# Kernel optimization log

Hardware: AMD Instinct MI355X
Metric: run time of the kernel (lower is better)

The kernel has to match this reference:

```python
import jax, jax.numpy as jnp
import numpy as np
from jax import lax

B, L, H = 32, 512, 1024
PRED_LEN = 32
LN_EPS = 1e-5


def setup_inputs() -> dict:
    key = jax.random.key(0)
    k1, k2, k3 = jax.random.split(key, 3)
    x = jax.random.normal(k1, (B, L, H), dtype=jnp.float32)
    # scale recurrent/input weights by 1/sqrt(H) so the linear recurrence stays finite
    Wxh = jax.random.normal(k2, (H, H), dtype=jnp.float32) / jnp.sqrt(jnp.float32(H))
    Whh = jax.random.normal(k3, (H, H), dtype=jnp.float32) / jnp.sqrt(jnp.float32(H))
    ln_w = jnp.ones((H,), dtype=jnp.float32)
    ln_b = jnp.zeros((H,), dtype=jnp.float32)
    return {"x": x, "Wxh": Wxh, "Whh": Whh, "ln_w": ln_w, "ln_b": ln_b, "pred_len": PRED_LEN}


def _layer_norm(y, w, b):
    mu = jnp.mean(y, axis=-1, keepdims=True)
    var = jnp.mean(jnp.square(y - mu), axis=-1, keepdims=True)
    return (y - mu) * lax.rsqrt(var + LN_EPS) * w + b


def reference(x, Wxh, Whh, ln_w, ln_b, pred_len):
    b, l, h = x.shape
    # precompute input projections for all timesteps: x_t @ Wxh^T (nn.Linear convention)
    xW = jnp.einsum('blh,kh->lbk', x, Wxh)  # [L, B, H]
    WhhT = Whh.T

    def rec_step(h_t, xw_t):
        h_t = xw_t + h_t @ WhhT
        return h_t, h_t

    h0 = jnp.zeros((b, h), dtype=x.dtype)
    h_last, rec = lax.scan(rec_step, h0, xW)
    rec = jnp.transpose(rec, (1, 0, 2))  # [B, L, H]

    def pred_step(h_t, _):
        h_t = h_t @ WhhT
        return h_t, h_t

    _, outs = lax.scan(pred_step, h_last, None, length=pred_len)
    outs = jnp.transpose(outs, (1, 0, 2))  # [B, pred_len, H]
    outputs = _layer_norm(outs, ln_w, ln_b)
    return rec, outputs
```

## Files before the change

### kernel.cpp

```cpp
#include <hip/hip_runtime.h>

#define BB 32
#define LL 512
#define HH 1024
#define PRED 32
#define C8 8
#define NC8 (LL / C8)
#define LN_EPS 1e-5f

typedef short bf16x8 __attribute__((ext_vector_type(8)));
typedef short s16x4  __attribute__((ext_vector_type(4)));
typedef float f32x4  __attribute__((ext_vector_type(4)));

static __device__ __forceinline__ void split3(float x, short& h, short& m, short& l) {
    unsigned u = __float_as_uint(x);
    unsigned rh = (u + 0x7fffu + ((u >> 16) & 1u)) & 0xffff0000u;
    h = (short)(rh >> 16);
    float x1 = x - __uint_as_float(rh);
    unsigned u1 = __float_as_uint(x1);
    unsigned rm = (u1 + 0x7fffu + ((u1 >> 16) & 1u)) & 0xffff0000u;
    m = (short)(rm >> 16);
    float x2 = x1 - __uint_as_float(rm);
    unsigned u2 = __float_as_uint(x2);
    unsigned rl = (u2 + 0x7fffu + ((u2 >> 16) & 1u)) & 0xffff0000u;
    l = (short)(rl >> 16);
}

static __device__ __forceinline__ void split2(float x, short& h, short& m) {
    unsigned u = __float_as_uint(x);
    unsigned rh = (u + 0x7fffu + ((u >> 16) & 1u)) & 0xffff0000u;
    h = (short)(rh >> 16);
    float x1 = x - __uint_as_float(rh);
    unsigned u1 = __float_as_uint(x1);
    unsigned rm = (u1 + 0x7fffu + ((u1 >> 16) & 1u)) & 0xffff0000u;
    m = (short)(rm >> 16);
}

#define MFMA6(ACC, AH, AM, AL, BH, BM, BL) \
    ACC = __builtin_amdgcn_mfma_f32_16x16x32_bf16(AL, BH, ACC, 0, 0, 0); \
    ACC = __builtin_amdgcn_mfma_f32_16x16x32_bf16(AH, BL, ACC, 0, 0, 0); \
    ACC = __builtin_amdgcn_mfma_f32_16x16x32_bf16(AM, BM, ACC, 0, 0, 0); \
    ACC = __builtin_amdgcn_mfma_f32_16x16x32_bf16(AM, BH, ACC, 0, 0, 0); \
    ACC = __builtin_amdgcn_mfma_f32_16x16x32_bf16(AH, BM, ACC, 0, 0, 0); \
    ACC = __builtin_amdgcn_mfma_f32_16x16x32_bf16(AH, BH, ACC, 0, 0, 0);

__global__ __launch_bounds__(256) void transpose_k(const float* __restrict__ in,
                                                   float* __restrict__ out) {
    __shared__ float tile[32][33];
    int bx = blockIdx.x * 32, by = blockIdx.y * 32;
    int tx = threadIdx.x, ty = threadIdx.y;
    #pragma unroll
    for (int i = 0; i < 32; i += 8)
        tile[ty + i][tx] = in[(size_t)(by + ty + i) * HH + bx + tx];
    __syncthreads();
    #pragma unroll
    for (int i = 0; i < 32; i += 8)
        out[(size_t)(bx + ty + i) * HH + by + tx] = tile[tx][ty + i];
}

__global__ __launch_bounds__(256) void split_a(const float* __restrict__ src, long sb, long sc,
                                               short* __restrict__ dst, long dsb, long dsc,
                                               long ps) {
    int r = blockIdx.y;
    const float* s = src + (long)(r & 31) * sb + (long)(r >> 5) * sc + threadIdx.x * 4;
    short* d = dst + (long)(r & 31) * dsb + (long)(r >> 5) * dsc + threadIdx.x * 4;
    float4 v = *(const float4*)s;
    float xs[4] = {v.x, v.y, v.z, v.w};
    s16x4 vh, vm, vl;
    #pragma unroll
    for (int j = 0; j < 4; ++j) {
        short h, m, l;
        split3(xs[j], h, m, l);
        vh[j] = h; vm[j] = m; vl[j] = l;
    }
    *(s16x4*)(d) = vh;
    *(s16x4*)(d + ps) = vm;
    *(s16x4*)(d + 2 * ps) = vl;
}

__global__ __launch_bounds__(256) void split_t(const float* __restrict__ in,
                                               short* __restrict__ out) {
    const size_t HM = (size_t)HH * HH;
    __shared__ float tile[32][33];
    int n0 = blockIdx.x * 32, k0 = blockIdx.y * 32;
    int tx = threadIdx.x, ty = threadIdx.y;
    #pragma unroll
    for (int i = 0; i < 32; i += 8)
        tile[ty + i][tx] = in[(size_t)(k0 + ty + i) * HH + n0 + tx];
    __syncthreads();
    #pragma unroll
    for (int i = 0; i < 32; i += 8) {
        float v = tile[tx][ty + i];
        short h, m, l;
        split3(v, h, m, l);
        size_t o = (size_t)(n0 + ty + i) * HH + k0 + tx;
        out[o] = h; out[HM + o] = m; out[2 * HM + o] = l;
    }
}

__global__ __launch_bounds__(256) void tr_splits(const short* __restrict__ in,
                                                 short* __restrict__ out) {
    const size_t HM = (size_t)HH * HH;
    __shared__ short tile[32][33];
    int p = blockIdx.z;
    int k0 = blockIdx.x * 32, n0 = blockIdx.y * 32;
    int tx = threadIdx.x, ty = threadIdx.y;
    #pragma unroll
    for (int i = 0; i < 32; i += 8)
        tile[ty + i][tx] = in[p * HM + (size_t)(n0 + ty + i) * HH + k0 + tx];
    __syncthreads();
    #pragma unroll
    for (int i = 0; i < 32; i += 8)
        out[p * HM + (size_t)(k0 + ty + i) * HH + n0 + tx] = tile[tx][ty + i];
}

__global__ __launch_bounds__(256) void copy_splits(const short* __restrict__ src,
                                                   short* __restrict__ dst, long ps) {
    size_t off = (size_t)blockIdx.x * HH + threadIdx.x * 4;
    *(s16x4*)(dst + off)          = *(const s16x4*)(src + off);
    *(s16x4*)(dst + ps + off)     = *(const s16x4*)(src + ps + off);
    *(s16x4*)(dst + 2 * ps + off) = *(const s16x4*)(src + 2 * ps + off);
}

__global__ __launch_bounds__(256) void gemm_mx(const float* __restrict__ A,
                                               const short* __restrict__ SB,
                                               float* __restrict__ C) {
    const size_t HM = (size_t)HH * HH;
    __shared__ __align__(16) short As2[2][128][40];
    __shared__ __align__(16) short Bs2[2][64][40];
    const int tid = threadIdx.x;
    const int lane = tid & 63;
    const int w = tid >> 6;
    const int n0 = blockIdx.x * 64;
    const int m0 = blockIdx.y * 128;
    const int ar = tid >> 1;
    const int akc = (tid & 1) * 16;
    const float* Arow = A + (size_t)(m0 + ar) * HH + akc;
    const int bp = tid >> 7;
    const int bnr = tid & 63;
    const int bkh = ((tid >> 6) & 1) * 16;
    const short* Brow = SB + bp * HM + (size_t)(n0 + bnr) * HH + bkh;
    const int fr = lane & 15;
    const int fk = (lane >> 4) * 8;

    f32x4 acc[2][4] = {};

    float4 av0 = *(const float4*)(Arow);
    float4 av1 = *(const float4*)(Arow + 4);
    float4 av2 = *(const float4*)(Arow + 8);
    float4 av3 = *(const float4*)(Arow + 12);
    bf16x8 rb0 = *(const bf16x8*)(Brow);
    bf16x8 rb1 = *(const bf16x8*)(Brow + 8);

    for (int kt = 0; kt < HH; kt += 32) {
        float xs[16] = {av0.x, av0.y, av0.z, av0.w, av1.x, av1.y, av1.z, av1.w,
                        av2.x, av2.y, av2.z, av2.w, av3.x, av3.y, av3.z, av3.w};
        bf16x8 vh0, vm0, vh1, vm1;
        #pragma unroll
        for (int j = 0; j < 8; ++j) {
            short h, m;
            split2(xs[j], h, m);
            vh0[j] = h; vm0[j] = m;
            split2(xs[j + 8], h, m);
            vh1[j] = h; vm1[j] = m;
        }
        *(bf16x8*)&As2[0][ar][akc]     = vh0;
        *(bf16x8*)&As2[0][ar][akc + 8] = vh1;
        *(bf16x8*)&As2[1][ar][akc]     = vm0;
        *(bf16x8*)&As2[1][ar][akc + 8] = vm1;
        *(bf16x8*)&Bs2[bp][bnr][bkh]     = rb0;
        *(bf16x8*)&Bs2[bp][bnr][bkh + 8] = rb1;
        __syncthreads();
        if (kt + 32 < HH) {
            const float* An = Arow + kt + 32;
            av0 = *(const float4*)(An);
            av1 = *(const float4*)(An + 4);
            av2 = *(const float4*)(An + 8);
            av3 = *(const float4*)(An + 12);
            const short* Bn = Brow + kt + 32;
            rb0 = *(const bf16x8*)(Bn);
            rb1 = *(const bf16x8*)(Bn + 8);
        }
        bf16x8 ah[2], am[2];
        #pragma unroll
        for (int i = 0; i < 2; ++i) {
            ah[i] = *(const bf16x8*)&As2[0][w * 32 + i * 16 + fr][fk];
            am[i] = *(const bf16x8*)&As2[1][w * 32 + i * 16 + fr][fk];
        }
        #pragma unroll
        for (int j = 0; j < 4; ++j) {
            bf16x8 bh = *(const bf16x8*)&Bs2[0][j * 16 + fr][fk];
            bf16x8 bm = *(const bf16x8*)&Bs2[1][j * 16 + fr][fk];
            #pragma unroll
            for (int i = 0; i < 2; ++i) {
                f32x4 a = acc[i][j];
                a = __builtin_amdgcn_mfma_f32_16x16x32_bf16(am[i], bm, a, 0, 0, 0);
                a = __builtin_amdgcn_mfma_f32_16x16x32_bf16(am[i], bh, a, 0, 0, 0);
                a = __builtin_amdgcn_mfma_f32_16x16x32_bf16(ah[i], bm, a, 0, 0, 0);
                a = __builtin_amdgcn_mfma_f32_16x16x32_bf16(ah[i], bh, a, 0, 0, 0);
                acc[i][j] = a;
            }
        }
        __syncthreads();
    }
    const int orow = (lane >> 4) * 4;
    #pragma unroll
    for (int i = 0; i < 2; ++i)
        #pragma unroll
        for (int j = 0; j < 4; ++j) {
            int c = n0 + j * 16 + fr;
            #pragma unroll
            for (int reg = 0; reg < 4; ++reg) {
                int r = m0 + w * 32 + i * 16 + orow + reg;
                C[(size_t)r * HH + c] = acc[i][j][reg];
            }
        }
}

struct GD  { const short* A; const short* B; float* O; float* P; short* S; };
struct GD8 { GD g[8]; };

__global__ __launch_bounds__(256) void step_b(
    GD8 dsc, int ypg,
    long sab, long sac, long psA,
    long sob, long soc, int add,
    long spb, long spc,
    long ssb, long ssc, long psS,
    int nrows) {
    const size_t HM = (size_t)HH * HH;
    __shared__ __align__(16) short As[3][128][40];
    __shared__ __align__(16) short Bs[3][64][40];
    const int tid = threadIdx.x;
    const int lane = tid & 63;
    const int w = tid >> 6;
    const int grp = blockIdx.y / ypg;
    const int yy  = blockIdx.y % ypg;
    const int n0 = blockIdx.x * 64;
    const int m0 = yy * 128;
    const GD d = dsc.g[grp];
    const int ar = tid >> 1;
    const int akh = (tid & 1) * 16;
    const int agr = m0 + ar;
    const short* Arow = d.A + (long)(agr & 31) * sab + (long)(agr >> 5) * sac + akh;
    const int br = tid >> 2;
    const int bkc = (tid & 3) * 8;
    const short* Brow = d.B + (size_t)(n0 + br) * HH + bkc;
    const int fr = lane & 15;
    const int fk = (lane >> 4) * 8;

    f32x4 acc[2][4] = {};

    bf16x8 ra[6], rb[3];
    #pragma unroll
    for (int p = 0; p < 3; ++p) {
        ra[2 * p]     = *(const bf16x8*)(Arow + p * psA);
        ra[2 * p + 1] = *(const bf16x8*)(Arow + p * psA + 8);
        rb[p]         = *(const bf16x8*)(Brow + p * HM);
    }
    for (int kt = 0; kt < HH; kt += 32) {
        #pragma unroll
        for (int p = 0; p < 3; ++p) {
            *(bf16x8*)&As[p][ar][akh]     = ra[2 * p];
            *(bf16x8*)&As[p][ar][akh + 8] = ra[2 * p + 1];
            *(bf16x8*)&Bs[p][br][bkc]     = rb[p];
        }
        __syncthreads();
        if (kt + 32 < HH) {
            #pragma unroll
            for (int p = 0; p < 3; ++p) {
                ra[2 * p]     = *(const bf16x8*)(Arow + p * psA + kt + 32);
                ra[2 * p + 1] = *(const bf16x8*)(Arow + p * psA + kt + 40);
                rb[p]         = *(const bf16x8*)(Brow + p * HM + kt + 32);
            }
        }
        bf16x8 af[3][2], bfr[3][4];
        #pragma unroll
        for (int p = 0; p < 3; ++p) {
            #pragma unroll
            for (int mf = 0; mf < 2; ++mf)
                af[p][mf] = *(const bf16x8*)&As[p][w * 32 + mf * 16 + fr][fk];
            #pragma unroll
            for (int nf = 0; nf < 4; ++nf)
                bfr[p][nf] = *(const bf16x8*)&Bs[p][nf * 16 + fr][fk];
        }
        #pragma unroll
        for (int mf = 0; mf < 2; ++mf)
            #pragma unroll
            for (int nf = 0; nf < 4; ++nf) {
                MFMA6(acc[mf][nf], af[0][mf], af[1][mf], af[2][mf],
                      bfr[0][nf], bfr[1][nf], bfr[2][nf])
            }
        __syncthreads();
    }
    const int orow = (lane >> 4) * 4;
    #pragma unroll
    for (int mf = 0; mf < 2; ++mf)
        #pragma unroll
        for (int nf = 0; nf < 4; ++nf) {
            int c = n0 + nf * 16 + fr;
            #pragma unroll
            for (int reg = 0; reg < 4; ++reg) {
                int r = m0 + w * 32 + mf * 16 + orow + reg;
                if (r >= nrows) continue;
                long rb_ = (long)(r & 31), rc_ = (long)(r >> 5);
                float val = acc[mf][nf][reg];
                if (d.O) {
                    float* p = d.O + rb_ * sob + rc_ * soc + c;
                    if (add) val += *p;
                    *p = val;
                }
                if (d.P) {
                    float* q = d.P + rb_ * spb + rc_ * spc + c;
                    *q += val;
                }
                if (d.S) {
                    short h, m, l;
                    split3(val, h, m, l);
                    short* s = d.S + rb_ * ssb + rc_ * ssc + c;
                    s[0] = h; s[psS] = m; s[2 * psS] = l;
                }
            }
        }
}

__global__ __launch_bounds__(128) void step_p(
    const short* __restrict__ SA, long sab, long sac, long psA,
    const short* __restrict__ SB,
    float* __restrict__ O, long sob, long soc, int add,
    float* __restrict__ P, long spb, long spc,
    short* __restrict__ S, long ssb, long ssc, long psS) {
    const size_t HM = (size_t)HH * HH;
    __shared__ __align__(16) short As[3][32][40];
    __shared__ __align__(16) short Bs[3][64][40];
    const int tid = threadIdx.x;
    const int lane = tid & 63;
    const int w = tid >> 6;
    const int n0 = blockIdx.x * 64;
    const int m0 = blockIdx.y * 32;
    const int ar = tid >> 2;
    const int akc = (tid & 3) * 8;
    const int agr = m0 + ar;
    const short* Arow = SA + (long)(agr & 31) * sab + (long)(agr >> 5) * sac + akc;
    const int bnr = tid & 63;
    const int bkh = (tid >> 6) * 16;
    const short* Brow = SB + (size_t)(n0 + bnr) * HH + bkh;
    const int fr = lane & 15;
    const int fk = (lane >> 4) * 8;
    f32x4 acc00 = 0, acc01 = 0, acc10 = 0, acc11 = 0;
    bf16x8 ra0 = *(const bf16x8*)(Arow);
    bf16x8 ra1 = *(const bf16x8*)(Arow + psA);
    bf16x8 ra2 = *(const bf16x8*)(Arow + 2 * psA);
    bf16x8 rb0 = *(const bf16x8*)(Brow);
    bf16x8 rb1 = *(const bf16x8*)(Brow + 8);
    bf16x8 rb2 = *(const bf16x8*)(Brow + HM);
    bf16x8 rb3 = *(const bf16x8*)(Brow + HM + 8);
    bf16x8 rb4 = *(const bf16x8*)(Brow + 2 * HM);
    bf16x8 rb5 = *(const bf16x8*)(Brow + 2 * HM + 8);
    for (int kt = 0; kt < HH; kt += 32) {
        *(bf16x8*)&As[0][ar][akc] = ra0;
        *(bf16x8*)&As[1][ar][akc] = ra1;
        *(bf16x8*)&As[2][ar][akc] = ra2;
        *(bf16x8*)&Bs[0][bnr][bkh] = rb0;
        *(bf16x8*)&Bs[0][bnr][bkh + 8] = rb1;
        *(bf16x8*)&Bs[1][bnr][bkh] = rb2;
        *(bf16x8*)&Bs[1][bnr][bkh + 8] = rb3;
        *(bf16x8*)&Bs[2][bnr][bkh] = rb4;
        *(bf16x8*)&Bs[2][bnr][bkh + 8] = rb5;
        __syncthreads();
        if (kt + 32 < HH) {
            const short* An = Arow + kt + 32;
            const short* Bn = Brow + kt + 32;
            ra0 = *(const bf16x8*)(An);
            ra1 = *(const bf16x8*)(An + psA);
            ra2 = *(const bf16x8*)(An + 2 * psA);
            rb0 = *(const bf16x8*)(Bn);
            rb1 = *(const bf16x8*)(Bn + 8);
            rb2 = *(const bf16x8*)(Bn + HM);
            rb3 = *(const bf16x8*)(Bn + HM + 8);
            rb4 = *(const bf16x8*)(Bn + 2 * HM);
            rb5 = *(const bf16x8*)(Bn + 2 * HM + 8);
        }
        bf16x8 a00 = *(const bf16x8*)&As[0][fr][fk];
        bf16x8 a01 = *(const bf16x8*)&As[0][16 + fr][fk];
        bf16x8 a10 = *(const bf16x8*)&As[1][fr][fk];
        bf16x8 a11 = *(const bf16x8*)&As[1][16 + fr][fk];
        bf16x8 a20 = *(const bf16x8*)&As[2][fr][fk];
        bf16x8 a21 = *(const bf16x8*)&As[2][16 + fr][fk];
        bf16x8 b00 = *(const bf16x8*)&Bs[0][w * 32 + fr][fk];
        bf16x8 b01 = *(const bf16x8*)&Bs[0][w * 32 + 16 + fr][fk];
        bf16x8 b10 = *(const bf16x8*)&Bs[1][w * 32 + fr][fk];
        bf16x8 b11 = *(const bf16x8*)&Bs[1][w * 32 + 16 + fr][fk];
        bf16x8 b20 = *(const bf16x8*)&Bs[2][w * 32 + fr][fk];
        bf16x8 b21 = *(const bf16x8*)&Bs[2][w * 32 + 16 + fr][fk];
        MFMA6(acc00, a00, a10, a20, b00, b10, b20)
        MFMA6(acc01, a00, a10, a20, b01, b11, b21)
        MFMA6(acc10, a01, a11, a21, b00, b10, b20)
        MFMA6(acc11, a01, a11, a21, b01, b11, b21)
        __syncthreads();
    }
    const int orow = (lane >> 4) * 4;
    #pragma unroll
    for (int mf = 0; mf < 2; ++mf) {
        #pragma unroll
        for (int nf = 0; nf < 2; ++nf) {
            f32x4 v = mf == 0 ? (nf == 0 ? acc00 : acc01) : (nf == 0 ? acc10 : acc11);
            int c = n0 + w * 32 + nf * 16 + fr;
            #pragma unroll
            for (int reg = 0; reg < 4; ++reg) {
                int r = m0 + mf * 16 + orow + reg;
                long rb = (long)(r & 31), rc = (long)(r >> 5);
                float val = v[reg];
                if (O) {
                    float* p = O + rb * sob + rc * soc + c;
                    if (add) val += *p;
                    *p = val;
                }
                if (P) { float* q = P + rb * spb + rc * spc + c; *q += val; }
                if (S) {
                    short h, m, l;
                    split3(val, h, m, l);
                    short* s = S + rb * ssb + rc * ssc + c;
                    s[0] = h; s[psS] = m; s[2 * psS] = l;
                }
            }
        }
    }
}

__global__ __launch_bounds__(256) void step_p64(
    const short* __restrict__ SA, long sab, long sac, long psA,
    const short* __restrict__ SB,
    float* __restrict__ O, long sob, long soc, int add,
    float* __restrict__ P, long spb, long spc,
    short* __restrict__ S, long ssb, long ssc, long psS,
    int nrows) {
    const size_t HM = (size_t)HH * HH;
    __shared__ __align__(16) short As[3][64][40];
    __shared__ __align__(16) short Bs[3][64][40];
    const int tid = threadIdx.x;
    const int lane = tid & 63;
    const int w = tid >> 6;
    const int wr = w & 1;
    const int wc = w >> 1;
    const int n0 = blockIdx.x * 64;
    const int m0 = blockIdx.y * 64;
    const int ar = tid >> 2;
    const int akc = (tid & 3) * 8;
    const int agr = m0 + ar;
    const short* Arow = SA + (long)(agr & 31) * sab + (long)(agr >> 5) * sac + akc;
    const short* Brow = SB + (size_t)(n0 + ar) * HH + akc;
    const int fr = lane & 15;
    const int fk = (lane >> 4) * 8;
    f32x4 acc00 = 0, acc01 = 0, acc10 = 0, acc11 = 0;
    bf16x8 ra0 = *(const bf16x8*)(Arow);
    bf16x8 ra1 = *(const bf16x8*)(Arow + psA);
    bf16x8 ra2 = *(const bf16x8*)(Arow + 2 * psA);
    bf16x8 rb0 = *(const bf16x8*)(Brow);
    bf16x8 rb1 = *(const bf16x8*)(Brow + HM);
    bf16x8 rb2 = *(const bf16x8*)(Brow + 2 * HM);
    for (int kt = 0; kt < HH; kt += 32) {
        *(bf16x8*)&As[0][ar][akc] = ra0;
        *(bf16x8*)&As[1][ar][akc] = ra1;
        *(bf16x8*)&As[2][ar][akc] = ra2;
        *(bf16x8*)&Bs[0][ar][akc] = rb0;
        *(bf16x8*)&Bs[1][ar][akc] = rb1;
        *(bf16x8*)&Bs[2][ar][akc] = rb2;
        __syncthreads();
        if (kt + 32 < HH) {
            const short* An = Arow + kt + 32;
            const short* Bn = Brow + kt + 32;
            ra0 = *(const bf16x8*)(An);
            ra1 = *(const bf16x8*)(An + psA);
            ra2 = *(const bf16x8*)(An + 2 * psA);
            rb0 = *(const bf16x8*)(Bn);
            rb1 = *(const bf16x8*)(Bn + HM);
            rb2 = *(const bf16x8*)(Bn + 2 * HM);
        }
        bf16x8 a00 = *(const bf16x8*)&As[0][wr * 32 + fr][fk];
        bf16x8 a01 = *(const bf16x8*)&As[0][wr * 32 + 16 + fr][fk];
        bf16x8 a10 = *(const bf16x8*)&As[1][wr * 32 + fr][fk];
        bf16x8 a11 = *(const bf16x8*)&As[1][wr * 32 + 16 + fr][fk];
        bf16x8 a20 = *(const bf16x8*)&As[2][wr * 32 + fr][fk];
        bf16x8 a21 = *(const bf16x8*)&As[2][wr * 32 + 16 + fr][fk];
        bf16x8 b00 = *(const bf16x8*)&Bs[0][wc * 32 + fr][fk];
        bf16x8 b01 = *(const bf16x8*)&Bs[0][wc * 32 + 16 + fr][fk];
        bf16x8 b10 = *(const bf16x8*)&Bs[1][wc * 32 + fr][fk];
        bf16x8 b11 = *(const bf16x8*)&Bs[1][wc * 32 + 16 + fr][fk];
        bf16x8 b20 = *(const bf16x8*)&Bs[2][wc * 32 + fr][fk];
        bf16x8 b21 = *(const bf16x8*)&Bs[2][wc * 32 + 16 + fr][fk];
        MFMA6(acc00, a00, a10, a20, b00, b10, b20)
        MFMA6(acc01, a00, a10, a20, b01, b11, b21)
        MFMA6(acc10, a01, a11, a21, b00, b10, b20)
        MFMA6(acc11, a01, a11, a21, b01, b11, b21)
        __syncthreads();
    }
    const int orow = (lane >> 4) * 4;
    #pragma unroll
    for (int mf = 0; mf < 2; ++mf) {
        #pragma unroll
        for (int nf = 0; nf < 2; ++nf) {
            f32x4 v = mf == 0 ? (nf == 0 ? acc00 : acc01) : (nf == 0 ? acc10 : acc11);
            int c = n0 + wc * 32 + nf * 16 + fr;
            #pragma unroll
            for (int reg = 0; reg < 4; ++reg) {
                int r = m0 + wr * 32 + mf * 16 + orow + reg;
                if (r >= nrows) continue;
                long rb = (long)(r & 31), rc = (long)(r >> 5);
                float val = v[reg];
                if (O) {
                    float* p = O + rb * sob + rc * soc + c;
                    if (add) val += *p;
                    *p = val;
                }
                if (P) { float* q = P + rb * spb + rc * spc + c; *q += val; }
                if (S) {
                    short h, m, l;
                    split3(val, h, m, l);
                    short* s = S + rb * ssb + rc * ssc + c;
                    s[0] = h; s[psS] = m; s[2 * psS] = l;
                }
            }
        }
    }
}

__global__ __launch_bounds__(512) void step_p128(
    const short* __restrict__ SA, long sab, long sac, long psA,
    const short* __restrict__ SB,
    float* __restrict__ O, long sob, long soc, int add,
    float* __restrict__ P, long spb, long spc,
    short* __restrict__ S, long ssb, long ssc, long psS,
    int nrows) {
    const size_t HM = (size_t)HH * HH;
    __shared__ __align__(16) short As[3][128][40];
    __shared__ __align__(16) short Bs[3][64][40];
    const int tid = threadIdx.x;
    const int lane = tid & 63;
    const int w = tid >> 6;
    const int wr = w & 3;
    const int wc = w >> 2;
    const int n0 = blockIdx.x * 64;
    const int m0 = blockIdx.y * 128;
    const int ar = tid >> 2;
    const int akc = (tid & 3) * 8;
    const int agr = m0 + ar;
    const short* Arow = SA + (long)(agr & 31) * sab + (long)(agr >> 5) * sac + akc;
    const bool bst = (tid < 384);
    const int bp = (tid >> 7) == 3 ? 2 : (tid >> 7);
    const int bt = tid & 127;
    const int bnr = bt >> 1;
    const int bkh = (bt & 1) * 16;
    const short* Brow = SB + (size_t)bp * HM + (size_t)(n0 + bnr) * HH + bkh;
    const int fr = lane & 15;
    const int fk = (lane >> 4) * 8;
    f32x4 acc00 = 0, acc01 = 0, acc10 = 0, acc11 = 0;
    bf16x8 ra0 = *(const bf16x8*)(Arow);
    bf16x8 ra1 = *(const bf16x8*)(Arow + psA);
    bf16x8 ra2 = *(const bf16x8*)(Arow + 2 * psA);
    bf16x8 rb0 = {}, rb1 = {};
    if (bst) { rb0 = *(const bf16x8*)(Brow); rb1 = *(const bf16x8*)(Brow + 8); }
    for (int kt = 0; kt < HH; kt += 32) {
        *(bf16x8*)&As[0][ar][akc] = ra0;
        *(bf16x8*)&As[1][ar][akc] = ra1;
        *(bf16x8*)&As[2][ar][akc] = ra2;
        if (bst) {
            *(bf16x8*)&Bs[bp][bnr][bkh]     = rb0;
            *(bf16x8*)&Bs[bp][bnr][bkh + 8] = rb1;
        }
        __syncthreads();
        if (kt + 32 < HH) {
            const short* An = Arow + kt + 32;
            ra0 = *(const bf16x8*)(An);
            ra1 = *(const bf16x8*)(An + psA);
            ra2 = *(const bf16x8*)(An + 2 * psA);
            if (bst) {
                const short* Bn = Brow + kt + 32;
                rb0 = *(const bf16x8*)(Bn);
                rb1 = *(const bf16x8*)(Bn + 8);
            }
        }
        bf16x8 a00 = *(const bf16x8*)&As[0][wr * 32 + fr][fk];
        bf16x8 a01 = *(const bf16x8*)&As[0][wr * 32 + 16 + fr][fk];
        bf16x8 a10 = *(const bf16x8*)&As[1][wr * 32 + fr][fk];
        bf16x8 a11 = *(const bf16x8*)&As[1][wr * 32 + 16 + fr][fk];
        bf16x8 a20 = *(const bf16x8*)&As[2][wr * 32 + fr][fk];
        bf16x8 a21 = *(const bf16x8*)&As[2][wr * 32 + 16 + fr][fk];
        bf16x8 b00 = *(const bf16x8*)&Bs[0][wc * 32 + fr][fk];
        bf16x8 b01 = *(const bf16x8*)&Bs[0][wc * 32 + 16 + fr][fk];
        bf16x8 b10 = *(const bf16x8*)&Bs[1][wc * 32 + fr][fk];
        bf16x8 b11 = *(const bf16x8*)&Bs[1][wc * 32 + 16 + fr][fk];
        bf16x8 b20 = *(const bf16x8*)&Bs[2][wc * 32 + fr][fk];
        bf16x8 b21 = *(const bf16x8*)&Bs[2][wc * 32 + 16 + fr][fk];
        MFMA6(acc00, a00, a10, a20, b00, b10, b20)
        MFMA6(acc01, a00, a10, a20, b01, b11, b21)
        MFMA6(acc10, a01, a11, a21, b00, b10, b20)
        MFMA6(acc11, a01, a11, a21, b01, b11, b21)
        __syncthreads();
    }
    const int orow = (lane >> 4) * 4;
    #pragma unroll
    for (int mf = 0; mf < 2; ++mf) {
        #pragma unroll
        for (int nf = 0; nf < 2; ++nf) {
            f32x4 v = mf == 0 ? (nf == 0 ? acc00 : acc01) : (nf == 0 ? acc10 : acc11);
            int c = n0 + wc * 32 + nf * 16 + fr;
            #pragma unroll
            for (int reg = 0; reg < 4; ++reg) {
                int r = m0 + wr * 32 + mf * 16 + orow + reg;
                if (r >= nrows) continue;
                long rb = (long)(r & 31), rc = (long)(r >> 5);
                float val = v[reg];
                if (O) {
                    float* p = O + rb * sob + rc * soc + c;
                    if (add) val += *p;
                    *p = val;
                }
                if (P) { float* q = P + rb * spb + rc * spc + c; *q += val; }
                if (S) {
                    short h, m, l;
                    split3(val, h, m, l);
                    short* s = S + rb * ssb + rc * ssc + c;
                    s[0] = h; s[psS] = m; s[2 * psS] = l;
                }
            }
        }
    }
}

__global__ __launch_bounds__(256) void ln_k(float* __restrict__ y,
                                            const float* __restrict__ w,
                                            const float* __restrict__ bia) {
    __shared__ float red[8];
    int row = blockIdx.x;
    float* p = y + (size_t)row * HH;
    int i4 = threadIdx.x * 4;
    float4 v = *(const float4*)&p[i4];
    float s = v.x + v.y + v.z + v.w;
    #pragma unroll
    for (int o = 32; o > 0; o >>= 1) s += __shfl_down(s, o, 64);
    int wid = threadIdx.x >> 6;
    if ((threadIdx.x & 63) == 0) red[wid] = s;
    __syncthreads();
    if (threadIdx.x == 0) red[4] = (red[0] + red[1] + red[2] + red[3]) * (1.f / HH);
    __syncthreads();
    float mu = red[4];
    float dx = v.x - mu, dy = v.y - mu, dz = v.z - mu, dw = v.w - mu;
    float q = dx * dx + dy * dy + dz * dz + dw * dw;
    #pragma unroll
    for (int o = 32; o > 0; o >>= 1) q += __shfl_down(q, o, 64);
    if ((threadIdx.x & 63) == 0) red[wid] = q;
    __syncthreads();
    if (threadIdx.x == 0) red[5] = (red[0] + red[1] + red[2] + red[3]) * (1.f / HH);
    __syncthreads();
    float rs = rsqrtf(red[5] + LN_EPS);
    float4 o4;
    o4.x = dx * rs * w[i4 + 0] + bia[i4 + 0];
    o4.y = dy * rs * w[i4 + 1] + bia[i4 + 1];
    o4.z = dz * rs * w[i4 + 2] + bia[i4 + 2];
    o4.w = dw * rs * w[i4 + 3] + bia[i4 + 3];
    *(float4*)&p[i4] = o4;
}

extern "C" void kernel_launch(void* const* d_in, const int* in_sizes, int n_in,
                              void* d_out, int out_size, void* d_ws, size_t ws_size,
                              hipStream_t stream) {
    const float* x    = (const float*)d_in[0];
    const float* Wxh  = (const float*)d_in[1];
    const float* Whh  = (const float*)d_in[2];
    const float* ln_w = (const float*)d_in[3];
    const float* ln_b = (const float*)d_in[4];

    const size_t MiB = 1024 * 1024;
    const long HM  = (long)HH * HH;
    const long PS2 = 2048L * HH;
    float* rec  = (float*)d_out;
    float* outp = rec + (size_t)BB * LL * HH;

    const long LH  = (long)LL * HH;
    const long CH8 = (long)C8 * HH;
    const long PB  = (long)PRED * HH;
    const long RS  = (long)HH;
    const long RC  = 32L * HH;
    float* nulf = (float*)nullptr;
    short* nuls = (short*)nullptr;
    char* wsb = (char*)d_ws;

    if (ws_size >= 124 * MiB) {
        float* TP   = (float*)(wsb);
        short* SBW  = (short*)(wsb + 4  * MiB);
        float* T3a  = (float*)(wsb + 4  * MiB);
        float* T3c  = (float*)(wsb + 8  * MiB);
        float* T3e  = (float*)(wsb + 12 * MiB);
        short* PW   = (short*)(wsb + 16 * MiB);
        const size_t PWs = 3 * (size_t)HH * HH;
        short* SB16 = (short*)(wsb + 64 * MiB);
        short* SC32 = (short*)(wsb + 70 * MiB);
        short* SC64 = (short*)(wsb + 76 * MiB);
        short* SC128= (short*)(wsb + 82 * MiB);
        short* SC256= (short*)(wsb + 88 * MiB);
        short* SA0  = (short*)(wsb + 94 * MiB);
        short* SA1  = (short*)(wsb + 106 * MiB);
        short* SAP = (short*)(wsb + 94 * MiB);
        short* SA2 = (short*)(wsb + 100 * MiB);
        short* SA4 = (short*)(wsb + 106 * MiB);
        short* SA6 = (short*)(wsb + 112 * MiB);

        GD8 D{};
        #define LAUNCH_B(NG, YPG, SAB, SAC, PSA, SOB, SOC, ADD, SPB, SPC, SSB, SSC, PSS, NR) \
            step_b<<<dim3(16, (NG) * (YPG)), 256, 0, stream>>>(D, YPG, \
                SAB, SAC, PSA, SOB, SOC, ADD, SPB, SPC, SSB, SSC, PSS, NR)
        #define G1(AA, BS, OO, SS) do { D.g[0] = {AA, BS, OO, nulf, SS}; } while (0)

        transpose_k<<<dim3(32, 32), dim3(32, 8), 0, stream>>>(Whh, TP);
        split_a<<<dim3(1, HH), 256, 0, stream>>>(Wxh, RS, RC, SBW, RS, RC, HM);
        gemm_mx<<<dim3(16, 128), 256, 0, stream>>>(x, SBW, rec);
        split_a<<<dim3(1, HH), 256, 0, stream>>>(TP, RS, RC, SAP, RS, RC, HM);
        split_t<<<dim3(32, 32), dim3(32, 8), 0, stream>>>(TP, PW);

        G1(SAP, PW, TP, SA2);  LAUNCH_B(1, 8, RS, RC, HM, RS, RC, 0, 0, 0, RS, RC, HM, 1024);
        split_t<<<dim3(32, 32), dim3(32, 8), 0, stream>>>(TP, PW + 1 * PWs);
        G1(SA2, PW + 1 * PWs, TP, SA4);  LAUNCH_B(1, 8, RS, RC, HM, RS, RC, 0, 0, 0, RS, RC, HM, 1024);
        split_t<<<dim3(32, 32), dim3(32, 8), 0, stream>>>(TP, PW + 3 * PWs);
        D.g[0] = {SA2, PW, T3a, nulf, nuls};
        D.g[1] = {SA4, PW, T3c, nulf, nuls};
        D.g[2] = {SA4, PW + 1 * PWs, T3e, nulf, SA6};
        LAUNCH_B(3, 8, RS, RC, HM, RS, RC, 0, 0, 0, RS, RC, HM, 1024);
        split_t<<<dim3(32, 32), dim3(32, 8), 0, stream>>>(T3a, PW + 2 * PWs);
        split_t<<<dim3(32, 32), dim3(32, 8), 0, stream>>>(T3c, PW + 4 * PWs);
        split_t<<<dim3(32, 32), dim3(32, 8), 0, stream>>>(T3e, PW + 5 * PWs);
        G1(SA6, PW, TP, nuls);  LAUNCH_B(1, 8, RS, RC, HM, RS, RC, 0, 0, 0, RS, RC, HM, 1024);
        split_t<<<dim3(32, 32), dim3(32, 8), 0, stream>>>(TP, PW + 6 * PWs);
        G1(SA4, PW + 3 * PWs, TP, SAP);  LAUNCH_B(1, 8, RS, RC, HM, RS, RC, 0, 0, 0, RS, RC, HM, 1024);
        split_t<<<dim3(32, 32), dim3(32, 8), 0, stream>>>(TP, PW + 7 * PWs);
        G1(SAP, PW + 7 * PWs, TP, SA2);  LAUNCH_B(1, 8, RS, RC, HM, RS, RC, 0, 0, 0, RS, RC, HM, 1024);
        split_t<<<dim3(32, 32), dim3(32, 8), 0, stream>>>(TP, SB16);
        G1(SA2, SB16, TP, SA4);  LAUNCH_B(1, 8, RS, RC, HM, RS, RC, 0, 0, 0, RS, RC, HM, 1024);
        split_t<<<dim3(32, 32), dim3(32, 8), 0, stream>>>(TP, SC32);
        G1(SA4, SC32, TP, SA2);  LAUNCH_B(1, 8, RS, RC, HM, RS, RC, 0, 0, 0, RS, RC, HM, 1024);
        split_t<<<dim3(32, 32), dim3(32, 8), 0, stream>>>(TP, SC64);
        G1(SA2, SC64, TP, SA4);  LAUNCH_B(1, 8, RS, RC, HM, RS, RC, 0, 0, 0, RS, RC, HM, 1024);
        split_t<<<dim3(32, 32), dim3(32, 8), 0, stream>>>(TP, SC128);
        G1(SA4, SC128, TP, nuls);  LAUNCH_B(1, 8, RS, RC, HM, RS, RC, 0, 0, 0, RS, RC, HM, 1024);
        split_t<<<dim3(32, 32), dim3(32, 8), 0, stream>>>(TP, SC256);

        split_a<<<dim3(1, 2048), 256, 0, stream>>>(rec, LH, CH8, SA0, RS, RC, PS2);
        for (int o = 1; o < C8; ++o) {
            short* Ain = (o & 1) ? SA0 : SA1;
            short* Sot = (o & 1) ? SA1 : SA0;
            step_p128<<<dim3(16, 16), 512, 0, stream>>>(Ain, RS, RC, PS2, PW,
                rec + (size_t)o * HH, LH, CH8, 1, nulf, 0, 0,
                Sot, RS, RC, PS2, 2048);
        }

        const short* SPOW[6] = {PW + 7 * PWs, SB16, SC32, SC64, SC128, SC256};
        short* SRC = SA1; short* DST = SA0;
        for (int s = 0; s < 6; ++s) {
            int T = 1 << s;
            int rows_ = (NC8 - T) * 32;
            step_p128<<<dim3(16, (rows_ + 127) / 128), 512, 0, stream>>>(
                SRC, RS, RC, PS2, SPOW[s],
                rec + (size_t)(T * C8 + C8 - 1) * HH, LH, CH8, 1,
                nulf, 0, 0, DST + (size_t)T * RC, RS, RC, PS2, rows_);
            copy_splits<<<T * 32, 256, 0, stream>>>(SRC, DST, PS2);
            short* t = SRC; SRC = DST; DST = t;
        }
        short* SFIN = SRC;
        short* SFREE = DST;

        for (int g = 0; g < 7; ++g)
            D.g[g] = {SFIN, PW + (size_t)g * PWs, nulf, rec + (size_t)(C8 + g) * HH, nuls};
        LAUNCH_B(7, 16, RS, RC, PS2, 0, 0, 0, LH, CH8, 0, 0, PS2, 2016);

        for (int g = 0; g < 8; ++g)
            D.g[g] = {SFIN + 63 * RC, PW + (size_t)g * PWs, outp + (size_t)g * HH,
                      nulf, SFREE + (size_t)g * RC};
        LAUNCH_B(8, 1, RS, 0, PS2, PB, 0, 0, 0, 0, RS, 0, PS2, 32);
        G1(SFREE, PW + 7 * PWs, outp + 8 * HH, SFREE + 8 * RC);
        LAUNCH_B(1, 2, RS, RC, PS2, PB, (long)HH, 0, 0, 0, RS, RC, PS2, 256);
        G1(SFREE, SB16, outp + 16 * HH, nuls);
        LAUNCH_B(1, 4, RS, RC, PS2, PB, (long)HH, 0, 0, 0, 0, 0, PS2, 512);
        #undef LAUNCH_B
        #undef G1

        ln_k<<<BB * PRED, 256, 0, stream>>>(outp, ln_w, ln_b);
        return;
    }

    {
        float* TP   = (float*)(wsb);
        short* SAP  = (short*)(wsb + 4 * MiB);
        short* SA0  = (short*)(wsb + 10 * MiB);
        short* SA1  = (short*)(wsb + 22 * MiB);
        short* SBM  = (short*)(wsb + 34 * MiB);
        short* SB8  = (short*)(wsb + 40 * MiB);
        short* SB16 = (short*)(wsb + 46 * MiB);
        short* SBr0 = (short*)(wsb + 52 * MiB);
        short* SBr1 = (short*)(wsb + 58 * MiB);

        transpose_k<<<dim3(32, 32), dim3(32, 8), 0, stream>>>(Whh, TP);
        split_a<<<dim3(1, HH), 256, 0, stream>>>(Wxh, RS, RC, SBr0, RS, RC, HM);
        gemm_mx<<<dim3(16, 128), 256, 0, stream>>>(x, SBr0, rec);
        split_a<<<dim3(1, HH), 256, 0, stream>>>(TP, RS, RC, SAP, RS, RC, HM);
        split_t<<<dim3(32, 32), dim3(32, 8), 0, stream>>>(TP, SBM);

        #define SQ64(SAi, SBi, Sot) \
            step_p64<<<dim3(16, 16), 256, 0, stream>>>(SAi, RS, RC, HM, SBi, \
                TP, RS, RC, 0, nulf, 0, 0, Sot, RS, RC, HM, 1024)
        SQ64(SAP, SBM, SA1);
        split_t<<<dim3(32, 32), dim3(32, 8), 0, stream>>>(TP, SBr0);
        SQ64(SA1, SBr0, SAP);
        split_t<<<dim3(32, 32), dim3(32, 8), 0, stream>>>(TP, SBr1);
        SQ64(SAP, SBr1, SA1);
        split_t<<<dim3(32, 32), dim3(32, 8), 0, stream>>>(TP, SB8);
        SQ64(SA1, SB8, SAP);
        split_t<<<dim3(32, 32), dim3(32, 8), 0, stream>>>(TP, SB16);

        split_a<<<dim3(1, 2048), 256, 0, stream>>>(rec, LH, CH8, SA0, RS, RC, PS2);
        for (int o = 1; o < C8; ++o) {
            short* Ain = (o & 1) ? SA0 : SA1;
            short* Sot = (o & 1) ? SA1 : SA0;
            step_p128<<<dim3(16, 16), 512, 0, stream>>>(Ain, RS, RC, PS2, SBM,
                rec + (size_t)o * HH, LH, CH8, 1, nulf, 0, 0,
                Sot, RS, RC, PS2, 2048);
        }
        #define SCAN(SRC, DST, T, SBpow) do { \
            int rows_ = (NC8 - (T)) * 32; \
            step_p128<<<dim3(16, (rows_ + 127) / 128), 512, 0, stream>>>( \
                SRC, RS, RC, PS2, SBpow, \
                rec + (size_t)((T) * C8 + C8 - 1) * HH, LH, CH8, 1, \
                nulf, 0, 0, DST + (size_t)(T) * RC, RS, RC, PS2, rows_); \
            copy_splits<<<(T) * 32, 256, 0, stream>>>(SRC, DST, PS2); \
        } while (0)
        #define SQI(SBi, SBo, last) do { \
            step_p64<<<dim3(16, 16), 256, 0, stream>>>(SAP, RS, RC, HM, SBi, \
                TP, RS, RC, 0, nulf, 0, 0, nuls, 0, 0, HM, 1024); \
            split_t<<<dim3(32, 32), dim3(32, 8), 0, stream>>>(TP, SBo); \
            if (!(last)) split_a<<<dim3(1, HH), 256, 0, stream>>>(TP, RS, RC, SAP, RS, RC, HM); \
        } while (0)
        SCAN(SA1, SA0, 1, SB8);
        SQI(SB16, SBr0, 0);
        SCAN(SA0, SA1, 2, SB16);
        SQI(SBr0, SBr1, 0);
        SCAN(SA1, SA0, 4, SBr0);
        SQI(SBr1, SBr0, 0);
        SCAN(SA0, SA1, 8, SBr1);
        SQI(SBr0, SBr1, 1);
        SCAN(SA1, SA0, 16, SBr0);
        SCAN(SA0, SA1, 32, SBr1);
        for (int o = 0; o < C8 - 1; ++o) {
            short* Ain = (o & 1) ? SA0 : SA1;
            short* Sot = (o & 1) ? SA1 : SA0;
            step_p128<<<dim3(16, 16), 512, 0, stream>>>(Ain, RS, RC, PS2, SBM,
                nulf, 0, 0, 0,
                rec + (size_t)(C8 + o) * HH, LH, CH8,
                (o == C8 - 2) ? nuls : Sot, RS, RC, PS2, 2016);
        }
        step_p<<<dim3(16, 1), 128, 0, stream>>>(SA1 + 63 * RC, RS, 0, PS2, SBM,
            outp, PB, 0, 0, nulf, 0, 0, SA0, RS, 0, PS2);
        step_p<<<dim3(16, 1), 128, 0, stream>>>(SA0, RS, 0, PS2, SBM,
            outp + HH, PB, 0, 0, nulf, 0, 0, SA0 + RC, RS, 0, PS2);
        tr_splits<<<dim3(32, 32, 3), dim3(32, 8), 0, stream>>>(SBM, SAP);
        SQ64(SAP, SBM, nuls);
        split_t<<<dim3(32, 32), dim3(32, 8), 0, stream>>>(TP, SBr0);
        step_p<<<dim3(16, 2), 128, 0, stream>>>(SA0, RS, RC, PS2, SBr0,
            outp + 2 * HH, PB, RS, 0, nulf, 0, 0,
            SA0 + 2 * RC, RS, RC, PS2);
        split_a<<<dim3(1, HH), 256, 0, stream>>>(TP, RS, RC, SAP, RS, RC, HM);
        SQ64(SAP, SBr0, nuls);
        split_t<<<dim3(32, 32), dim3(32, 8), 0, stream>>>(TP, SBr1);
        step_p<<<dim3(16, 4), 128, 0, stream>>>(SA0, RS, RC, PS2, SBr1,
            outp + 4 * HH, PB, RS, 0, nulf, 0, 0,
            SA0 + 4 * RC, RS, RC, PS2);
        step_p<<<dim3(16, 8), 128, 0, stream>>>(SA0, RS, RC, PS2, SB8,
            outp + 8 * HH, PB, RS, 0, nulf, 0, 0,
            SA0 + 8 * RC, RS, RC, PS2);
        step_p64<<<dim3(16, 8), 256, 0, stream>>>(SA0, RS, RC, PS2, SB16,
            outp + 16 * HH, PB, RS, 0, nulf, 0, 0,
            nuls, 0, 0, PS2, 512);
        #undef SQ64
        #undef SCAN
        #undef SQI

        ln_k<<<BB * PRED, 256, 0, stream>>>(outp, ln_w, ln_b);
    }
}
```

Measured before the change: 1.498 ms.

## Fuse matrix-power precomputation into chunk recurrence launches via heterogeneous grouped GEMM

Replaces the serial chain of standalone Whh power squarings (each with its own split_t transpose pass) with a grouped GEMM kernel whose groups carry per-group strides and row ranges. The power products are computed alongside the per-chunk recurrence GEMMs in the same launch, so the small 8-block power GEMMs fill otherwise idle CUs instead of running on the critical path. Powers are stored directly in split bf16 form as both A (Whh^k) and B (transposed) operands, which removes the transpose and split kernels. The cost is a larger descriptor, a group-lookup loop per block, and a heavier per-block kernel (256 threads, 128 rows) in place of step_p128 for the recurrence steps.

Result: faster. 1.323 ms (-11.7%).

```diff
diff --git a/kernel.cpp b/kernel.cpp
--- a/kernel.cpp
+++ b/kernel.cpp
@@ -217,36 +217,36 @@
         }
 }
 
-struct GD  { const short* A; const short* B; float* O; float* P; short* S; };
-struct GD8 { GD g[8]; };
-
-__global__ __launch_bounds__(256) void step_b(
-    GD8 dsc, int ypg,
-    long sab, long sac, long psA,
-    long sob, long soc, int add,
-    long spb, long spc,
-    long ssb, long ssc, long psS,
-    int nrows) {
+struct GDv {
+    const short* A; const short* B; float* O; float* P; short* S;
+    int sab, sac, psA, sob, soc, spb, spc, ssb, ssc, psS, add, nrows, ybeg;
+};
+struct GDv8 { GDv g[8]; };
+
+__global__ __launch_bounds__(256) void step_g(GDv8 dsc, int ng) {
     const size_t HM = (size_t)HH * HH;
     __shared__ __align__(16) short As[3][128][40];
     __shared__ __align__(16) short Bs[3][64][40];
     const int tid = threadIdx.x;
     const int lane = tid & 63;
     const int w = tid >> 6;
-    const int grp = blockIdx.y / ypg;
-    const int yy  = blockIdx.y % ypg;
+    const int yy = blockIdx.y;
+    int gi = 0;
+    for (int i = 1; i < ng; ++i)
+        if (yy >= dsc.g[i].ybeg) gi = i;
+    const GDv d = dsc.g[gi];
     const int n0 = blockIdx.x * 64;
-    const int m0 = yy * 128;
-    const GD d = dsc.g[grp];
+    const int m0 = (yy - d.ybeg) * 128;
     const int ar = tid >> 1;
     const int akh = (tid & 1) * 16;
     const int agr = m0 + ar;
-    const short* Arow = d.A + (long)(agr & 31) * sab + (long)(agr >> 5) * sac + akh;
+    const short* Arow = d.A + (long)(agr & 31) * d.sab + (long)(agr >> 5) * d.sac + akh;
     const int br = tid >> 2;
     const int bkc = (tid & 3) * 8;
     const short* Brow = d.B + (size_t)(n0 + br) * HH + bkc;
     const int fr = lane & 15;
     const int fk = (lane >> 4) * 8;
+    const long psA = d.psA;
 
     f32x4 acc[2][4] = {};
 
@@ -301,23 +301,23 @@
             #pragma unroll
             for (int reg = 0; reg < 4; ++reg) {
                 int r = m0 + w * 32 + mf * 16 + orow + reg;
-                if (r >= nrows) continue;
+                if (r >= d.nrows) continue;
                 long rb_ = (long)(r & 31), rc_ = (long)(r >> 5);
                 float val = acc[mf][nf][reg];
                 if (d.O) {
-                    float* p = d.O + rb_ * sob + rc_ * soc + c;
-                    if (add) val += *p;
+                    float* p = d.O + rb_ * d.sob + rc_ * d.soc + c;
+                    if (d.add) val += *p;
                     *p = val;
                 }
                 if (d.P) {
-                    float* q = d.P + rb_ * spb + rc_ * spc + c;
+                    float* q = d.P + rb_ * d.spb + rc_ * d.spc + c;
                     *q += val;
                 }
                 if (d.S) {
                     short h, m, l;
                     split3(val, h, m, l);
-                    short* s = d.S + rb_ * ssb + rc_ * ssc + c;
-                    s[0] = h; s[psS] = m; s[2 * psS] = l;
+                    short* s = d.S + rb_ * d.ssb + rc_ * d.ssc + c;
+                    s[0] = h; s[d.psS] = m; s[2 * (long)d.psS] = l;
                 }
             }
         }
@@ -686,101 +686,154 @@
     char* wsb = (char*)d_ws;
 
     if (ws_size >= 124 * MiB) {
-        float* TP   = (float*)(wsb);
-        short* SBW  = (short*)(wsb + 4  * MiB);
-        float* T3a  = (float*)(wsb + 4  * MiB);
-        float* T3c  = (float*)(wsb + 8  * MiB);
-        float* T3e  = (float*)(wsb + 12 * MiB);
-        short* PW   = (short*)(wsb + 16 * MiB);
-        const size_t PWs = 3 * (size_t)HH * HH;
-        short* SB16 = (short*)(wsb + 64 * MiB);
-        short* SC32 = (short*)(wsb + 70 * MiB);
-        short* SC64 = (short*)(wsb + 76 * MiB);
-        short* SC128= (short*)(wsb + 82 * MiB);
-        short* SC256= (short*)(wsb + 88 * MiB);
-        short* SA0  = (short*)(wsb + 94 * MiB);
-        short* SA1  = (short*)(wsb + 106 * MiB);
-        short* SAP = (short*)(wsb + 94 * MiB);
-        short* SA2 = (short*)(wsb + 100 * MiB);
-        short* SA4 = (short*)(wsb + 106 * MiB);
-        short* SA6 = (short*)(wsb + 112 * MiB);
-
-        GD8 D{};
-        #define LAUNCH_B(NG, YPG, SAB, SAC, PSA, SOB, SOC, ADD, SPB, SPC, SSB, SSC, PSS, NR) \
-            step_b<<<dim3(16, (NG) * (YPG)), 256, 0, stream>>>(D, YPG, \
-                SAB, SAC, PSA, SOB, SOC, ADD, SPB, SPC, SSB, SSC, PSS, NR)
-        #define G1(AA, BS, OO, SS) do { D.g[0] = {AA, BS, OO, nulf, SS}; } while (0)
-
-        transpose_k<<<dim3(32, 32), dim3(32, 8), 0, stream>>>(Whh, TP);
+        auto NA = [&](int idx) -> short* { return (short*)wsb + (size_t)idx * 3 * HM; };
+        short* MAs[3] = {(short*)(wsb + 78 * MiB), (short*)(wsb + 84 * MiB),
+                         (short*)(wsb + 90 * MiB)};
+        short* SA0 = (short*)(wsb + 96 * MiB);
+        short* SA1 = (short*)(wsb + 108 * MiB);
+        short* SBW = SA0;
+        float* TPf = (float*)SA1;
+
+        GDv8 D{};
+        auto launch = [&](int ng, int ytot) {
+            step_g<<<dim3(16, ytot), 256, 0, stream>>>(D, ng);
+        };
+        auto g_sq = [&](const short* A_, const short* B_, short* S_, int ybeg) -> GDv {
+            GDv v{};
+            v.A = A_; v.B = B_; v.O = nullptr; v.P = nullptr; v.S = S_;
+            v.sab = HH; v.sac = 32 * HH; v.psA = (int)HM;
+            v.ssb = HH; v.ssc = 32 * HH; v.psS = (int)HM;
+            v.add = 0; v.nrows = 1024; v.ybeg = ybeg;
+            return v;
+        };
+
+        transpose_k<<<dim3(32, 32), dim3(32, 8), 0, stream>>>(Whh, TPf);
+        split_a<<<dim3(1, HH), 256, 0, stream>>>(Whh, RS, RC, NA(0), RS, RC, HM);
+        split_a<<<dim3(1, HH), 256, 0, stream>>>(TPf, RS, RC, MAs[0], RS, RC, HM);
         split_a<<<dim3(1, HH), 256, 0, stream>>>(Wxh, RS, RC, SBW, RS, RC, HM);
         gemm_mx<<<dim3(16, 128), 256, 0, stream>>>(x, SBW, rec);
-        split_a<<<dim3(1, HH), 256, 0, stream>>>(TP, RS, RC, SAP, RS, RC, HM);
-        split_t<<<dim3(32, 32), dim3(32, 8), 0, stream>>>(TP, PW);
-
-        G1(SAP, PW, TP, SA2);  LAUNCH_B(1, 8, RS, RC, HM, RS, RC, 0, 0, 0, RS, RC, HM, 1024);
-        split_t<<<dim3(32, 32), dim3(32, 8), 0, stream>>>(TP, PW + 1 * PWs);
-        G1(SA2, PW + 1 * PWs, TP, SA4);  LAUNCH_B(1, 8, RS, RC, HM, RS, RC, 0, 0, 0, RS, RC, HM, 1024);
-        split_t<<<dim3(32, 32), dim3(32, 8), 0, stream>>>(TP, PW + 3 * PWs);
-        D.g[0] = {SA2, PW, T3a, nulf, nuls};
-        D.g[1] = {SA4, PW, T3c, nulf, nuls};
-        D.g[2] = {SA4, PW + 1 * PWs, T3e, nulf, SA6};
-        LAUNCH_B(3, 8, RS, RC, HM, RS, RC, 0, 0, 0, RS, RC, HM, 1024);
-        split_t<<<dim3(32, 32), dim3(32, 8), 0, stream>>>(T3a, PW + 2 * PWs);
-        split_t<<<dim3(32, 32), dim3(32, 8), 0, stream>>>(T3c, PW + 4 * PWs);
-        split_t<<<dim3(32, 32), dim3(32, 8), 0, stream>>>(T3e, PW + 5 * PWs);
-        G1(SA6, PW, TP, nuls);  LAUNCH_B(1, 8, RS, RC, HM, RS, RC, 0, 0, 0, RS, RC, HM, 1024);
-        split_t<<<dim3(32, 32), dim3(32, 8), 0, stream>>>(TP, PW + 6 * PWs);
-        G1(SA4, PW + 3 * PWs, TP, SAP);  LAUNCH_B(1, 8, RS, RC, HM, RS, RC, 0, 0, 0, RS, RC, HM, 1024);
-        split_t<<<dim3(32, 32), dim3(32, 8), 0, stream>>>(TP, PW + 7 * PWs);
-        G1(SAP, PW + 7 * PWs, TP, SA2);  LAUNCH_B(1, 8, RS, RC, HM, RS, RC, 0, 0, 0, RS, RC, HM, 1024);
-        split_t<<<dim3(32, 32), dim3(32, 8), 0, stream>>>(TP, SB16);
-        G1(SA2, SB16, TP, SA4);  LAUNCH_B(1, 8, RS, RC, HM, RS, RC, 0, 0, 0, RS, RC, HM, 1024);
-        split_t<<<dim3(32, 32), dim3(32, 8), 0, stream>>>(TP, SC32);
-        G1(SA4, SC32, TP, SA2);  LAUNCH_B(1, 8, RS, RC, HM, RS, RC, 0, 0, 0, RS, RC, HM, 1024);
-        split_t<<<dim3(32, 32), dim3(32, 8), 0, stream>>>(TP, SC64);
-        G1(SA2, SC64, TP, SA4);  LAUNCH_B(1, 8, RS, RC, HM, RS, RC, 0, 0, 0, RS, RC, HM, 1024);
-        split_t<<<dim3(32, 32), dim3(32, 8), 0, stream>>>(TP, SC128);
-        G1(SA4, SC128, TP, nuls);  LAUNCH_B(1, 8, RS, RC, HM, RS, RC, 0, 0, 0, RS, RC, HM, 1024);
-        split_t<<<dim3(32, 32), dim3(32, 8), 0, stream>>>(TP, SC256);
 
         split_a<<<dim3(1, 2048), 256, 0, stream>>>(rec, LH, CH8, SA0, RS, RC, PS2);
+        short* SAc = SA0;
+        short* SAn = SA1;
         for (int o = 1; o < C8; ++o) {
-            short* Ain = (o & 1) ? SA0 : SA1;
-            short* Sot = (o & 1) ? SA1 : SA0;
-            step_p128<<<dim3(16, 16), 512, 0, stream>>>(Ain, RS, RC, PS2, PW,
-                rec + (size_t)o * HH, LH, CH8, 1, nulf, 0, 0,
-                Sot, RS, RC, PS2, 2048);
-        }
-
-        const short* SPOW[6] = {PW + 7 * PWs, SB16, SC32, SC64, SC128, SC256};
-        short* SRC = SA1; short* DST = SA0;
+            GDv mn{};
+            mn.A = SAc; mn.B = NA(0);
+            mn.O = rec + (size_t)o * HH; mn.sob = (int)LH; mn.soc = (int)CH8; mn.add = 1;
+            mn.P = nullptr; mn.S = SAn;
+            mn.sab = HH; mn.sac = 32 * HH; mn.psA = (int)PS2;
+            mn.ssb = HH; mn.ssc = 32 * HH; mn.psS = (int)PS2;
+            mn.nrows = 2048; mn.ybeg = 0;
+            D.g[0] = mn;
+            int ng = 1, yt = 16;
+            auto add_sq = [&](const short* A_, const short* B_, short* S_) {
+                D.g[ng++] = g_sq(A_, B_, S_, yt); yt += 8;
+            };
+            switch (o) {
+                case 1:
+                    add_sq(MAs[0], NA(0), MAs[1]);
+                    add_sq(NA(0), MAs[0], NA(1));
+                    break;
+                case 2:
+                    add_sq(MAs[1], NA(1), MAs[2]);
+                    add_sq(NA(1), MAs[0], NA(2));
+                    add_sq(NA(1), MAs[1], NA(3));
+                    break;
+                case 3:
+                    add_sq(NA(3), MAs[0], NA(4));
+                    add_sq(NA(3), MAs[1], NA(5));
+                    add_sq(NA(3), MAs[2], NA(7));
+                    break;
+                case 4:
+                    add_sq(NA(2), MAs[2], NA(6));
+                    add_sq(MAs[2], NA(3), MAs[0]);
+                    break;
+                case 5:
+                    add_sq(NA(7), MAs[0], NA(8));
+                    add_sq(MAs[0], NA(7), MAs[1]);
+                    break;
+                case 6:
+                    add_sq(NA(8), MAs[1], NA(9));
+                    add_sq(MAs[1], NA(8), MAs[2]);
+                    break;
+                case 7:
+                    add_sq(NA(9), MAs[2], NA(10));
+                    add_sq(MAs[2], NA(9), MAs[0]);
+                    break;
+            }
+            launch(ng, yt);
+            short* t = SAc; SAc = SAn; SAn = t;
+        }
+
+        short* SRC = SAc;
+        short* DST = SAn;
         for (int s = 0; s < 6; ++s) {
             int T = 1 << s;
             int rows_ = (NC8 - T) * 32;
-            step_p128<<<dim3(16, (rows_ + 127) / 128), 512, 0, stream>>>(
-                SRC, RS, RC, PS2, SPOW[s],
-                rec + (size_t)(T * C8 + C8 - 1) * HH, LH, CH8, 1,
-                nulf, 0, 0, DST + (size_t)T * RC, RS, RC, PS2, rows_);
+            int yb = (rows_ + 127) / 128;
+            GDv mn{};
+            mn.A = SRC; mn.B = NA(s == 0 ? 7 : 7 + s);
+            mn.O = rec + (size_t)(T * C8 + C8 - 1) * HH;
+            mn.sob = (int)LH; mn.soc = (int)CH8; mn.add = 1;
+            mn.P = nullptr; mn.S = DST + (size_t)T * RC;
+            mn.sab = HH; mn.sac = 32 * HH; mn.psA = (int)PS2;
+            mn.ssb = HH; mn.ssc = 32 * HH; mn.psS = (int)PS2;
+            mn.nrows = rows_; mn.ybeg = 0;
+            D.g[0] = mn;
+            int ng = 1, yt = yb;
+            if (s == 0) {
+                D.g[ng++] = g_sq(NA(10), MAs[0], NA(11), yt); yt += 8;
+                D.g[ng++] = g_sq(MAs[0], NA(10), MAs[1], yt); yt += 8;
+            } else if (s == 1) {
+                D.g[ng++] = g_sq(NA(11), MAs[1], NA(12), yt); yt += 8;
+            }
+            launch(ng, yt);
             copy_splits<<<T * 32, 256, 0, stream>>>(SRC, DST, PS2);
             short* t = SRC; SRC = DST; DST = t;
         }
         short* SFIN = SRC;
         short* SFREE = DST;
 
-        for (int g = 0; g < 7; ++g)
-            D.g[g] = {SFIN, PW + (size_t)g * PWs, nulf, rec + (size_t)(C8 + g) * HH, nuls};
-        LAUNCH_B(7, 16, RS, RC, PS2, 0, 0, 0, LH, CH8, 0, 0, PS2, 2016);
-
-        for (int g = 0; g < 8; ++g)
-            D.g[g] = {SFIN + 63 * RC, PW + (size_t)g * PWs, outp + (size_t)g * HH,
-                      nulf, SFREE + (size_t)g * RC};
-        LAUNCH_B(8, 1, RS, 0, PS2, PB, 0, 0, 0, 0, RS, 0, PS2, 32);
-        G1(SFREE, PW + 7 * PWs, outp + 8 * HH, SFREE + 8 * RC);
-        LAUNCH_B(1, 2, RS, RC, PS2, PB, (long)HH, 0, 0, 0, RS, RC, PS2, 256);
-        G1(SFREE, SB16, outp + 16 * HH, nuls);
-        LAUNCH_B(1, 4, RS, RC, PS2, PB, (long)HH, 0, 0, 0, 0, 0, PS2, 512);
-        #undef LAUNCH_B
-        #undef G1
+        for (int g = 0; g < 7; ++g) {
+            GDv v{};
+            v.A = SFIN; v.B = NA(g);
+            v.O = nullptr; v.S = nullptr;
+            v.P = rec + (size_t)(C8 + g) * HH;
+            v.spb = (int)LH; v.spc = (int)CH8;
+            v.sab = HH; v.sac = 32 * HH; v.psA = (int)PS2;
+            v.nrows = 2016; v.ybeg = g * 16;
+            D.g[g] = v;
+        }
+        launch(7, 112);
+
+        for (int g = 0; g < 8; ++g) {
+            GDv v{};
+            v.A = SFIN + 63 * RC; v.B = NA(g);
+            v.O = outp + (size_t)g * HH; v.sob = (int)PB; v.soc = 0; v.add = 0;
+            v.P = nullptr;
+            v.S = SFREE + (size_t)g * RC; v.ssb = HH; v.ssc = 0; v.psS = (int)PS2;
+            v.sab = HH; v.sac = 0; v.psA = (int)PS2;
+            v.nrows = 32; v.ybeg = g;
+            D.g[g] = v;
+        }
+        launch(8, 8);
+        {
+            GDv v{};
+            v.A = SFREE; v.B = NA(7);
+            v.O = outp + 8 * HH; v.sob = (int)PB; v.soc = HH; v.add = 0;
+            v.P = nullptr;
+            v.S = SFREE + 8 * RC; v.ssb = HH; v.ssc = 32 * HH; v.psS = (int)PS2;
+            v.sab = HH; v.sac = 32 * HH; v.psA = (int)PS2;
+            v.nrows = 256; v.ybeg = 0;
+            D.g[0] = v;
+            launch(1, 2);
+            v.B = NA(8);
+            v.O = outp + 16 * HH;
+            v.S = nullptr;
+            v.nrows = 512;
+            D.g[0] = v;
+            launch(1, 4);
+        }
 
         ln_k<<<BB * PRED, 256, 0, stream>>>(outp, ln_w, ln_b);
         return;
```
